# Performance work log

Measured on AMD Instinct MI355X. Metric: run time of the kernel, lower is better.

## Reference

```python
import jax, jax.numpy as jnp
import numpy as np

H = W = 28
NUM_COUNTS = 10  # iteration counts 0..9, one per logit of determine_n


def conv2d(x, w, b=None, pad=2):
    # x: [B,C,H,W], w: [O,I,5,5]
    y = jax.lax.conv_general_dilated(
        x, w, window_strides=(1, 1), padding=[(pad, pad), (pad, pad)],
        dimension_numbers=("NCHW", "OIHW", "NCHW"))
    if b is not None:
        y = y + b[None, :, None, None]
    return y


def maxpool3(x):
    # kernel 3, stride 3, valid: 28 -> 9
    return jax.lax.reduce_window(
        x, -jnp.inf, jax.lax.max,
        window_dimensions=(1, 1, 3, 3), window_strides=(1, 1, 3, 3),
        padding="VALID")


def setup_inputs() -> dict:
    key = jax.random.key(0)
    ks = jax.random.split(key, 8)
    B = 4096
    s = 0.1
    return {
        "x": jax.random.normal(ks[0], (B, H * W), dtype=jnp.float32),
        "w1": jax.random.normal(ks[1], (8, 1, 5, 5), dtype=jnp.float32) * s,
        "b1": jax.random.normal(ks[2], (8,), dtype=jnp.float32) * s,
        "w2": jax.random.normal(ks[3], (16, 8, 5, 5), dtype=jnp.float32) * s,
        "b2": jax.random.normal(ks[4], (16,), dtype=jnp.float32) * s,
        "fcw": jax.random.normal(ks[5], (10, 16 * 9 * 9), dtype=jnp.float32) * s,
        "fcb": jax.random.normal(ks[6], (10,), dtype=jnp.float32) * s,
        "iterw": jax.random.normal(ks[7], (1, 1, 5, 5), dtype=jnp.float32) * s,
    }


def reference(x, w1, b1, w2, b2, fcw, fcb, iterw):
    B = x.shape[0]
    xi = x.reshape(B, 1, H, W)
    # determine_n: CNN router producing 10 logits over iteration counts
    h = jax.nn.relu(conv2d(xi, w1, b1))
    h = jax.nn.relu(conv2d(h, w2, b2))
    h = maxpool3(h).reshape(B, -1)                      # [B, 1296]
    logits = h @ fcw.T + fcb                            # [B, 10]
    probs = jax.nn.softmax(logits, axis=-1)             # [B, 10]
    # smooth TmIter: expected value over f^n(base), n = 0..9
    def step(y, _):
        return conv2d(y, iterw, None), y
    _, ys = jax.lax.scan(step, xi, None, length=NUM_COUNTS)  # [10,B,1,28,28]
    out = jnp.einsum("bn,nbchw->bchw", probs, ys)
    return out.reshape(B, H, W)
```

## Files before the change

kernel.cpp:

```cpp
#include <hip/hip_runtime.h>
#include <hip/hip_bf16.h>
#include <math.h>
#include <float.h>

typedef __fp16 f16x8  __attribute__((ext_vector_type(8)));
typedef float  f32x16 __attribute__((ext_vector_type(16)));
typedef float  f32x4  __attribute__((ext_vector_type(4)));
typedef float  f32x2  __attribute__((ext_vector_type(2)));

#define DY_TAB 0xA524A509A502A540ULL
#define DX_TAB 0x446A444A44924924ULL

__global__ __launch_bounds__(256, 4) void k1_router(
    const float* __restrict__ xg,
    const float* __restrict__ w1g,
    const float* __restrict__ b1g,
    const float* __restrict__ w2g,
    const float* __restrict__ b2g,
    const float* __restrict__ fcwg,
    const float* __restrict__ fcbg,
    float* __restrict__ wsp)
{
    __shared__ __align__(16) char lds[28528];
    float*  spad   = (float*)(lds + 0);
    __fp16* sh1T   = (__fp16*)(lds + 4608);
    __fp16* sw2t   = (__fp16*)(lds + 21968);
    float*  pooled = (float*)(lds + 21968);
    float*  swred  = (float*)(lds + 28368);

    const int tid  = threadIdx.x;
    const int b    = blockIdx.x;
    const int lane = tid & 63;
    const int wid  = tid >> 6;

    const int ct = wid * 49 + lane;
    const int yy = ct / 7, q = ct - yy * 7;

    f32x4 z4 = {0.f, 0.f, 0.f, 0.f};
    for (int i = tid; i < 92; i += 256) {
        int row, cu;
        if (i < 36) { int r = i / 9; cu = i - 9 * r; row = r < 2 ? r : 28 + r; }
        else        { int j = i - 36; row = 2 + (j >> 1); cu = (j & 1) << 3; }
        ((f32x4*)spad)[row * 9 + cu] = z4;
    }
    for (int i = tid; i < 189; i += 256) {
        int row, col;
        if (i < 105) { int r = i / 35; row = (r == 2) ? 30 : r; col = i - 35 * r; }
        else         { int j = i - 105; row = 2 + j / 3; int cm = j - 3 * (j / 3);
                       col = (cm == 2) ? 30 : cm; }
        ((f32x4*)sh1T)[row * 35 + col] = z4;
    }
    for (int i = tid; i < 400; i += 256) {
        const int tap = i >> 4, ch = i & 15;
        f16x8 v;
        #pragma unroll
        for (int j = 0; j < 8; ++j) v[j] = (__fp16)w2g[ch * 200 + j * 25 + tap];
        *((f16x8*)(sw2t + i * 8)) = v;
    }
    if (lane < 49) {
        f32x4 v = *((const f32x4*)(xg + (size_t)b * 784 + yy * 28 + q * 4));
        *((f32x4*)(spad + (yy + 2) * 36 + q * 4 + 4)) = v;
    }
    __syncthreads();

    if (lane < 49) {
        float o[8][4];
        #pragma unroll
        for (int c = 0; c < 8; ++c) {
            const float bv = b1g[c];
            #pragma unroll
            for (int px = 0; px < 4; ++px) o[c][px] = bv;
        }
        #pragma unroll
        for (int r = 0; r < 5; ++r) {
            const float* rowp = spad + (yy + r) * 36 + q * 4;
            f32x4 a0 = ((const f32x4*)rowp)[0];
            f32x4 a1 = ((const f32x4*)rowp)[1];
            f32x4 a2 = ((const f32x4*)rowp)[2];
            float u[12] = {a0[0],a0[1],a0[2],a0[3], a1[0],a1[1],a1[2],a1[3],
                           a2[0],a2[1],a2[2],a2[3]};
            #pragma unroll
            for (int c = 0; c < 8; ++c)
                #pragma unroll
                for (int kx = 0; kx < 5; ++kx) {
                    const float w = w1g[c * 25 + r * 5 + kx];
                    #pragma unroll
                    for (int px = 0; px < 4; ++px)
                        o[c][px] = fmaf(u[2 + px + kx], w, o[c][px]);
                }
        }
        #pragma unroll
        for (int px = 0; px < 4; ++px) {
            f16x8 hv;
            #pragma unroll
            for (int c = 0; c < 8; ++c) hv[c] = (__fp16)fmaxf(o[c][px], 0.f);
            *((f16x8*)(sh1T + ((yy + 2) * 35 + (q * 4 + px + 2)) * 8)) = hv;
        }
    }
    const int lr = lane & 31;
    const int g2 = lane >> 5;
    int band = (lr * 57) >> 9; band = band > 2 ? 2 : band;
    const int dy = (int)((DY_TAB >> (2 * lr)) & 3ull);
    const int dx = (int)((DX_TAB >> (2 * lr)) & 3ull);
    const float biasv = (lr < 16) ? b2g[lr] : 0.f;

    f16x8 bfrag[13];
    int   toffB[13];
    #pragma unroll
    for (int s = 0; s < 13; ++s) {
        const int tap = 2 * s + g2;
        const int tapc = tap > 24 ? 24 : tap;
        f16x8 v = *((const f16x8*)(sw2t + (tapc * 16 + (lr & 15)) * 8));
        if (tap > 24 || lr >= 16) {
            #pragma unroll
            for (int j = 0; j < 8; ++j) v[j] = (__fp16)0.f;
        }
        bfrag[s] = v;
        const int ky = (tapc * 13) >> 6;
        const int kx = tapc - 5 * ky;
        toffB[s] = (ky * 35 + kx) * 16;
    }
    __syncthreads();

    for (int tile = wid; tile < 27; tile += 4) {
        const int cell = tile * 3 + band;
        const int cy = (cell * 57) >> 9, cx = cell - 9 * cy;
        const int R0 = 3 * cy + dy, C0 = 3 * cx + dx;
        const char* abase = (const char*)sh1T + (R0 * 35 + C0) * 16;
        f32x16 acc;
        #pragma unroll
        for (int r = 0; r < 16; ++r) acc[r] = biasv;
        #pragma unroll
        for (int s = 0; s < 13; ++s) {
            f16x8 af = *((const f16x8*)(abase + toffB[s]));
            acc = __builtin_amdgcn_mfma_f32_32x32x16_f16(af, bfrag[s], acc, 0, 0, 0);
        }
        float mA, mB, mC;
        if (g2 == 0) {
            mA = fmaxf(fmaxf(fmaxf(acc[0],acc[1]),fmaxf(acc[2],acc[3])), acc[4]);
            mB = fmaxf(fmaxf(fmaxf(acc[5],acc[6]),acc[7]), fmaxf(acc[8],acc[9]));
            mC = fmaxf(fmaxf(fmaxf(acc[10],acc[11]),acc[12]), fmaxf(acc[13],acc[14]));
        } else {
            mA = fmaxf(fmaxf(acc[0],acc[1]),fmaxf(acc[2],acc[3]));
            mB = fmaxf(fmaxf(acc[4],acc[5]),fmaxf(acc[6],acc[7]));
            mC = fmaxf(fmaxf(acc[8],acc[9]),fmaxf(acc[10],acc[11]));
        }
        mA = fmaxf(mA, 0.f); mB = fmaxf(mB, 0.f); mC = fmaxf(mC, 0.f);
        mA = fmaxf(mA, __shfl_xor(mA, 32, 64));
        mB = fmaxf(mB, __shfl_xor(mB, 32, 64));
        mC = fmaxf(mC, __shfl_xor(mC, 32, 64));
        if (g2 == 0 && lr < 16) {
            pooled[lr * 81 + tile * 3 + 0] = mA;
            pooled[lr * 81 + tile * 3 + 1] = mB;
            pooled[lr * 81 + tile * 3 + 2] = mC;
        }
    }
    __syncthreads();

    {
        float part[10];
        #pragma unroll
        for (int j = 0; j < 10; ++j) part[j] = 0.f;
        const int i4e = wid * 81 + 81;
        for (int i4 = wid * 81 + lane; i4 < i4e; i4 += 64) {
            const f32x4 pv = ((const f32x4*)pooled)[i4];
            #pragma unroll
            for (int j = 0; j < 10; ++j) {
                const f32x4 fw = *((const f32x4*)(fcwg + j * 1296 + i4 * 4));
                part[j] = fmaf(pv[0], fw[0], part[j]);
                part[j] = fmaf(pv[1], fw[1], part[j]);
                part[j] = fmaf(pv[2], fw[2], part[j]);
                part[j] = fmaf(pv[3], fw[3], part[j]);
            }
        }
        #pragma unroll
        for (int j = 0; j < 10; ++j) {
            float v = part[j];
            #pragma unroll
            for (int off = 32; off > 0; off >>= 1) v += __shfl_down(v, off, 64);
            if (lane == 0) swred[wid * 10 + j] = v;
        }
    }
    __syncthreads();

    if (tid == 0) {
        float lg[10]; float mx = -FLT_MAX;
        #pragma unroll
        for (int j = 0; j < 10; ++j) {
            lg[j] = swred[j] + swred[10 + j] + swred[20 + j] + swred[30 + j] + fcbg[j];
            mx = fmaxf(mx, lg[j]);
        }
        float sum = 0.f; float e[10];
        #pragma unroll
        for (int j = 0; j < 10; ++j) { e[j] = expf(lg[j] - mx); sum += e[j]; }
        const float inv = 1.f / sum;
        #pragma unroll
        for (int j = 0; j < 10; ++j) wsp[(size_t)b * 16 + j] = e[j] * inv;
    }
}

typedef __fp16 f16x2  __attribute__((ext_vector_type(2)));
typedef unsigned int u32x2 __attribute__((ext_vector_type(2)));

__device__ inline f16x2 as_h2(unsigned u) { union { unsigned x; f16x2 h; } c; c.x = u; return c.h; }
__device__ inline unsigned pack2(float lo, float hi) {
    union { f16x2 h; unsigned x; } c; c.h[0] = (__fp16)lo; c.h[1] = (__fp16)hi; return c.x;
}
__device__ inline float dot2f(unsigned a, unsigned b, float acc) {
#if __has_builtin(__builtin_amdgcn_fdot2)
    return __builtin_amdgcn_fdot2(as_h2(a), as_h2(b), acc, false);
#else
    f16x2 ah = as_h2(a), bh = as_h2(b);
    return fmaf((float)ah[1], (float)bh[1], fmaf((float)ah[0], (float)bh[0], acc));
#endif
}
#define ALIGN16(hi, lo) __builtin_amdgcn_alignbit((hi), (lo), 16)

__global__ __launch_bounds__(64, 4) void k2_scan(
    const float* __restrict__ xg,
    const float* __restrict__ iwg,
    const float* __restrict__ wsp,
    float* __restrict__ outg)
{
    __shared__ __align__(16) char arena[5120];
    char* bufA = arena;
    char* bufB = arena + 2560;

    const int tid = threadIdx.x;
    const int b   = blockIdx.x;

    f32x4 z4 = {0.f, 0.f, 0.f, 0.f};
    for (int i = tid; i < 320; i += 64) ((f32x4*)arena)[i] = z4;
    __syncthreads();

    for (int i = tid; i < 196; i += 64) {
        const int yy = i / 7, q = i - yy * 7;
        f32x4 v = *((const f32x4*)(xg + (size_t)b * 784 + yy * 28 + q * 4));
        unsigned* dst = (unsigned*)(bufA + (yy + 2) * 80 + q * 8 + 4);
        dst[0] = pack2(v[0], v[1]); dst[1] = pack2(v[2], v[3]);
    }
    __syncthreads();

    unsigned wp[5][3];
    #pragma unroll
    for (int r = 0; r < 5; ++r) {
        wp[r][0] = pack2(iwg[r * 5 + 0], iwg[r * 5 + 1]);
        wp[r][1] = pack2(iwg[r * 5 + 2], iwg[r * 5 + 3]);
        wp[r][2] = pack2(iwg[r * 5 + 4], 0.f);
    }

    const int rq = tid / 7, qq = tid - rq * 7;
    const float p0 = wsp[(size_t)b * 16];
    float accv[16];
    #pragma unroll
    for (int i = 0; i < 16; ++i) accv[i] = 0.f;

    const char* cur = bufA;
    char* nxt = bufB;
    #pragma unroll 1
    for (int n = 1; n <= 9; ++n) {
        const float pn = wsp[(size_t)b * 16 + n];
        if (tid < 49) {
            float v[4][4];
            #pragma unroll
            for (int rr = 0; rr < 4; ++rr)
                #pragma unroll
                for (int px = 0; px < 4; ++px) v[rr][px] = 0.f;
            #pragma unroll
            for (int r = 0; r < 8; ++r) {
                const char* rowb = cur + (4 * rq + r) * 80 + qq * 8;
                u32x2 A = *((const u32x2*)rowb);
                u32x2 B = *((const u32x2*)(rowb + 8));
                unsigned C0 = *((const unsigned*)(rowb + 16));
                unsigned P[8] = { A.x, ALIGN16(A.y, A.x), A.y, ALIGN16(B.x, A.y),
                                  B.x, ALIGN16(B.y, B.x), B.y, ALIGN16(C0,  B.y) };
                if (n == 1 && r >= 2 && r <= 5) {
                    f16x2 t1 = as_h2(A.y), t2 = as_h2(B.x);
                    accv[(r - 2) * 4 + 0] = p0 * (float)t1[0];
                    accv[(r - 2) * 4 + 1] = p0 * (float)t1[1];
                    accv[(r - 2) * 4 + 2] = p0 * (float)t2[0];
                    accv[(r - 2) * 4 + 3] = p0 * (float)t2[1];
                }
                #pragma unroll
                for (int rr = 0; rr < 4; ++rr) {
                    if (rr <= r && r <= rr + 4) {
                        const int ky = r - rr;
                        #pragma unroll
                        for (int px = 0; px < 4; ++px) {
                            float t = v[rr][px];
                            t = dot2f(P[px],     wp[ky][0], t);
                            t = dot2f(P[px + 2], wp[ky][1], t);
                            t = dot2f(P[px + 4], wp[ky][2], t);
                            v[rr][px] = t;
                        }
                    }
                }
            }
            if (n < 9) {
                #pragma unroll
                for (int rr = 0; rr < 4; ++rr) {
                    unsigned* dst = (unsigned*)(nxt + (4 * rq + rr + 2) * 80 + qq * 8 + 4);
                    dst[0] = pack2(v[rr][0], v[rr][1]);
                    dst[1] = pack2(v[rr][2], v[rr][3]);
                }
            }
            #pragma unroll
            for (int rr = 0; rr < 4; ++rr)
                #pragma unroll
                for (int px = 0; px < 4; ++px)
                    accv[rr * 4 + px] = fmaf(pn, v[rr][px], accv[rr * 4 + px]);
        }
        if (n < 9) __syncthreads();
        const char* t = cur; cur = nxt; nxt = (char*)t;
    }

    if (tid < 49) {
        #pragma unroll
        for (int rr = 0; rr < 4; ++rr) {
            f32x4 o = {accv[rr*4], accv[rr*4+1], accv[rr*4+2], accv[rr*4+3]};
            *((f32x4*)(outg + (size_t)b * 784 + (4 * rq + rr) * 28 + qq * 4)) = o;
        }
    }
}

extern "C" void kernel_launch(void* const* d_in, const int* in_sizes, int n_in,
                              void* d_out, int out_size, void* d_ws, size_t ws_size,
                              hipStream_t stream) {
    const float* x   = (const float*)d_in[0];
    const float* w1  = (const float*)d_in[1];
    const float* b1  = (const float*)d_in[2];
    const float* w2  = (const float*)d_in[3];
    const float* b2  = (const float*)d_in[4];
    const float* fcw = (const float*)d_in[5];
    const float* fcb = (const float*)d_in[6];
    const float* iw  = (const float*)d_in[7];
    float* out = (float*)d_out;
    float* wsp = (float*)d_ws;
    const int B = in_sizes[0] / 784;
    k1_router<<<B, 256, 0, stream>>>(x, w1, b1, w2, b2, fcw, fcb, wsp);
    k2_scan<<<B, 64, 0, stream>>>(x, iw, wsp, out);
}
```

Before: 113.8 us.

## Fuse router and iterative-conv scan into a single kernel

Merges the CNN router kernel and the 10-step iterated-convolution kernel into one 256-thread kernel per sample. The softmax probabilities now stay in shared memory instead of going through a global workspace, and the scan's input image is packed from the router's already-staged LDS copy rather than reloaded from global memory. This removes one kernel launch and the global round-trip. In exchange, the scan phase runs inside a 256-thread block where only the first wave does useful work, and each block holds the router's larger LDS footprint, which may lower occupancy during the scan.

```diff
diff --git a/kernel.cpp b/kernel.cpp
--- a/kernel.cpp
+++ b/kernel.cpp
@@ -4,202 +4,9 @@
 #include <float.h>
 
 typedef __fp16 f16x8  __attribute__((ext_vector_type(8)));
+typedef __fp16 f16x2  __attribute__((ext_vector_type(2)));
 typedef float  f32x16 __attribute__((ext_vector_type(16)));
 typedef float  f32x4  __attribute__((ext_vector_type(4)));
-typedef float  f32x2  __attribute__((ext_vector_type(2)));
-
-#define DY_TAB 0xA524A509A502A540ULL
-#define DX_TAB 0x446A444A44924924ULL
-
-__global__ __launch_bounds__(256, 4) void k1_router(
-    const float* __restrict__ xg,
-    const float* __restrict__ w1g,
-    const float* __restrict__ b1g,
-    const float* __restrict__ w2g,
-    const float* __restrict__ b2g,
-    const float* __restrict__ fcwg,
-    const float* __restrict__ fcbg,
-    float* __restrict__ wsp)
-{
-    __shared__ __align__(16) char lds[28528];
-    float*  spad   = (float*)(lds + 0);
-    __fp16* sh1T   = (__fp16*)(lds + 4608);
-    __fp16* sw2t   = (__fp16*)(lds + 21968);
-    float*  pooled = (float*)(lds + 21968);
-    float*  swred  = (float*)(lds + 28368);
-
-    const int tid  = threadIdx.x;
-    const int b    = blockIdx.x;
-    const int lane = tid & 63;
-    const int wid  = tid >> 6;
-
-    const int ct = wid * 49 + lane;
-    const int yy = ct / 7, q = ct - yy * 7;
-
-    f32x4 z4 = {0.f, 0.f, 0.f, 0.f};
-    for (int i = tid; i < 92; i += 256) {
-        int row, cu;
-        if (i < 36) { int r = i / 9; cu = i - 9 * r; row = r < 2 ? r : 28 + r; }
-        else        { int j = i - 36; row = 2 + (j >> 1); cu = (j & 1) << 3; }
-        ((f32x4*)spad)[row * 9 + cu] = z4;
-    }
-    for (int i = tid; i < 189; i += 256) {
-        int row, col;
-        if (i < 105) { int r = i / 35; row = (r == 2) ? 30 : r; col = i - 35 * r; }
-        else         { int j = i - 105; row = 2 + j / 3; int cm = j - 3 * (j / 3);
-                       col = (cm == 2) ? 30 : cm; }
-        ((f32x4*)sh1T)[row * 35 + col] = z4;
-    }
-    for (int i = tid; i < 400; i += 256) {
-        const int tap = i >> 4, ch = i & 15;
-        f16x8 v;
-        #pragma unroll
-        for (int j = 0; j < 8; ++j) v[j] = (__fp16)w2g[ch * 200 + j * 25 + tap];
-        *((f16x8*)(sw2t + i * 8)) = v;
-    }
-    if (lane < 49) {
-        f32x4 v = *((const f32x4*)(xg + (size_t)b * 784 + yy * 28 + q * 4));
-        *((f32x4*)(spad + (yy + 2) * 36 + q * 4 + 4)) = v;
-    }
-    __syncthreads();
-
-    if (lane < 49) {
-        float o[8][4];
-        #pragma unroll
-        for (int c = 0; c < 8; ++c) {
-            const float bv = b1g[c];
-            #pragma unroll
-            for (int px = 0; px < 4; ++px) o[c][px] = bv;
-        }
-        #pragma unroll
-        for (int r = 0; r < 5; ++r) {
-            const float* rowp = spad + (yy + r) * 36 + q * 4;
-            f32x4 a0 = ((const f32x4*)rowp)[0];
-            f32x4 a1 = ((const f32x4*)rowp)[1];
-            f32x4 a2 = ((const f32x4*)rowp)[2];
-            float u[12] = {a0[0],a0[1],a0[2],a0[3], a1[0],a1[1],a1[2],a1[3],
-                           a2[0],a2[1],a2[2],a2[3]};
-            #pragma unroll
-            for (int c = 0; c < 8; ++c)
-                #pragma unroll
-                for (int kx = 0; kx < 5; ++kx) {
-                    const float w = w1g[c * 25 + r * 5 + kx];
-                    #pragma unroll
-                    for (int px = 0; px < 4; ++px)
-                        o[c][px] = fmaf(u[2 + px + kx], w, o[c][px]);
-                }
-        }
-        #pragma unroll
-        for (int px = 0; px < 4; ++px) {
-            f16x8 hv;
-            #pragma unroll
-            for (int c = 0; c < 8; ++c) hv[c] = (__fp16)fmaxf(o[c][px], 0.f);
-            *((f16x8*)(sh1T + ((yy + 2) * 35 + (q * 4 + px + 2)) * 8)) = hv;
-        }
-    }
-    const int lr = lane & 31;
-    const int g2 = lane >> 5;
-    int band = (lr * 57) >> 9; band = band > 2 ? 2 : band;
-    const int dy = (int)((DY_TAB >> (2 * lr)) & 3ull);
-    const int dx = (int)((DX_TAB >> (2 * lr)) & 3ull);
-    const float biasv = (lr < 16) ? b2g[lr] : 0.f;
-
-    f16x8 bfrag[13];
-    int   toffB[13];
-    #pragma unroll
-    for (int s = 0; s < 13; ++s) {
-        const int tap = 2 * s + g2;
-        const int tapc = tap > 24 ? 24 : tap;
-        f16x8 v = *((const f16x8*)(sw2t + (tapc * 16 + (lr & 15)) * 8));
-        if (tap > 24 || lr >= 16) {
-            #pragma unroll
-            for (int j = 0; j < 8; ++j) v[j] = (__fp16)0.f;
-        }
-        bfrag[s] = v;
-        const int ky = (tapc * 13) >> 6;
-        const int kx = tapc - 5 * ky;
-        toffB[s] = (ky * 35 + kx) * 16;
-    }
-    __syncthreads();
-
-    for (int tile = wid; tile < 27; tile += 4) {
-        const int cell = tile * 3 + band;
-        const int cy = (cell * 57) >> 9, cx = cell - 9 * cy;
-        const int R0 = 3 * cy + dy, C0 = 3 * cx + dx;
-        const char* abase = (const char*)sh1T + (R0 * 35 + C0) * 16;
-        f32x16 acc;
-        #pragma unroll
-        for (int r = 0; r < 16; ++r) acc[r] = biasv;
-        #pragma unroll
-        for (int s = 0; s < 13; ++s) {
-            f16x8 af = *((const f16x8*)(abase + toffB[s]));
-            acc = __builtin_amdgcn_mfma_f32_32x32x16_f16(af, bfrag[s], acc, 0, 0, 0);
-        }
-        float mA, mB, mC;
-        if (g2 == 0) {
-            mA = fmaxf(fmaxf(fmaxf(acc[0],acc[1]),fmaxf(acc[2],acc[3])), acc[4]);
-            mB = fmaxf(fmaxf(fmaxf(acc[5],acc[6]),acc[7]), fmaxf(acc[8],acc[9]));
-            mC = fmaxf(fmaxf(fmaxf(acc[10],acc[11]),acc[12]), fmaxf(acc[13],acc[14]));
-        } else {
-            mA = fmaxf(fmaxf(acc[0],acc[1]),fmaxf(acc[2],acc[3]));
-            mB = fmaxf(fmaxf(acc[4],acc[5]),fmaxf(acc[6],acc[7]));
-            mC = fmaxf(fmaxf(acc[8],acc[9]),fmaxf(acc[10],acc[11]));
-        }
-        mA = fmaxf(mA, 0.f); mB = fmaxf(mB, 0.f); mC = fmaxf(mC, 0.f);
-        mA = fmaxf(mA, __shfl_xor(mA, 32, 64));
-        mB = fmaxf(mB, __shfl_xor(mB, 32, 64));
-        mC = fmaxf(mC, __shfl_xor(mC, 32, 64));
-        if (g2 == 0 && lr < 16) {
-            pooled[lr * 81 + tile * 3 + 0] = mA;
-            pooled[lr * 81 + tile * 3 + 1] = mB;
-            pooled[lr * 81 + tile * 3 + 2] = mC;
-        }
-    }
-    __syncthreads();
-
-    {
-        float part[10];
-        #pragma unroll
-        for (int j = 0; j < 10; ++j) part[j] = 0.f;
-        const int i4e = wid * 81 + 81;
-        for (int i4 = wid * 81 + lane; i4 < i4e; i4 += 64) {
-            const f32x4 pv = ((const f32x4*)pooled)[i4];
-            #pragma unroll
-            for (int j = 0; j < 10; ++j) {
-                const f32x4 fw = *((const f32x4*)(fcwg + j * 1296 + i4 * 4));
-                part[j] = fmaf(pv[0], fw[0], part[j]);
-                part[j] = fmaf(pv[1], fw[1], part[j]);
-                part[j] = fmaf(pv[2], fw[2], part[j]);
-                part[j] = fmaf(pv[3], fw[3], part[j]);
-            }
-        }
-        #pragma unroll
-        for (int j = 0; j < 10; ++j) {
-            float v = part[j];
-            #pragma unroll
-            for (int off = 32; off > 0; off >>= 1) v += __shfl_down(v, off, 64);
-            if (lane == 0) swred[wid * 10 + j] = v;
-        }
-    }
-    __syncthreads();
-
-    if (tid == 0) {
-        float lg[10]; float mx = -FLT_MAX;
-        #pragma unroll
-        for (int j = 0; j < 10; ++j) {
-            lg[j] = swred[j] + swred[10 + j] + swred[20 + j] + swred[30 + j] + fcbg[j];
-            mx = fmaxf(mx, lg[j]);
-        }
-        float sum = 0.f; float e[10];
-        #pragma unroll
-        for (int j = 0; j < 10; ++j) { e[j] = expf(lg[j] - mx); sum += e[j]; }
-        const float inv = 1.f / sum;
-        #pragma unroll
-        for (int j = 0; j < 10; ++j) wsp[(size_t)b * 16 + j] = e[j] * inv;
-    }
-}
-
-typedef __fp16 f16x2  __attribute__((ext_vector_type(2)));
 typedef unsigned int u32x2 __attribute__((ext_vector_type(2)));
 
 __device__ inline f16x2 as_h2(unsigned u) { union { unsigned x; f16x2 h; } c; c.x = u; return c.h; }
@@ -216,28 +23,206 @@
 }
 #define ALIGN16(hi, lo) __builtin_amdgcn_alignbit((hi), (lo), 16)
 
-__global__ __launch_bounds__(64, 4) void k2_scan(
+#define DY_TAB 0xA524A509A502A540ULL
+#define DX_TAB 0x446A444A44924924ULL
+
+__global__ __launch_bounds__(256, 4) void fused(
     const float* __restrict__ xg,
+    const float* __restrict__ w1g,
+    const float* __restrict__ b1g,
+    const float* __restrict__ w2g,
+    const float* __restrict__ b2g,
+    const float* __restrict__ fcwg,
+    const float* __restrict__ fcbg,
     const float* __restrict__ iwg,
-    const float* __restrict__ wsp,
     float* __restrict__ outg)
 {
-    __shared__ __align__(16) char arena[5120];
-    char* bufA = arena;
-    char* bufB = arena + 2560;
-
-    const int tid = threadIdx.x;
-    const int b   = blockIdx.x;
+    __shared__ __align__(16) char lds[28528];
+    float*  spad   = (float*)(lds + 0);
+    __fp16* sh1T   = (__fp16*)(lds + 4608);
+    char*   scanA  = lds + 4608;
+    char*   scanB  = lds + 7168;
+    __fp16* sw2t   = (__fp16*)(lds + 21968);
+    float*  pooled = (float*)(lds + 21968);
+    float*  swred  = (float*)(lds + 28368);
+
+    const int tid  = threadIdx.x;
+    const int b    = blockIdx.x;
+    const int lane = tid & 63;
+    const int wid  = tid >> 6;
+
+    const int ct = wid * 49 + lane;
+    const int yy = ct / 7, q = ct - yy * 7;
 
     f32x4 z4 = {0.f, 0.f, 0.f, 0.f};
-    for (int i = tid; i < 320; i += 64) ((f32x4*)arena)[i] = z4;
-    __syncthreads();
-
-    for (int i = tid; i < 196; i += 64) {
-        const int yy = i / 7, q = i - yy * 7;
+    for (int i = tid; i < 92; i += 256) {
+        int row, cu;
+        if (i < 36) { int r = i / 9; cu = i - 9 * r; row = r < 2 ? r : 28 + r; }
+        else        { int j = i - 36; row = 2 + (j >> 1); cu = (j & 1) << 3; }
+        ((f32x4*)spad)[row * 9 + cu] = z4;
+    }
+    for (int i = tid; i < 189; i += 256) {
+        int row, col;
+        if (i < 105) { int r = i / 35; row = (r == 2) ? 30 : r; col = i - 35 * r; }
+        else         { int j = i - 105; row = 2 + j / 3; int cm = j - 3 * (j / 3);
+                       col = (cm == 2) ? 30 : cm; }
+        ((f32x4*)sh1T)[row * 35 + col] = z4;
+    }
+    for (int i = tid; i < 400; i += 256) {
+        const int tap = i >> 4, ch = i & 15;
+        f16x8 v;
+        #pragma unroll
+        for (int j = 0; j < 8; ++j) v[j] = (__fp16)w2g[ch * 200 + j * 25 + tap];
+        *((f16x8*)(sw2t + i * 8)) = v;
+    }
+    if (lane < 49) {
         f32x4 v = *((const f32x4*)(xg + (size_t)b * 784 + yy * 28 + q * 4));
-        unsigned* dst = (unsigned*)(bufA + (yy + 2) * 80 + q * 8 + 4);
+        *((f32x4*)(spad + (yy + 2) * 36 + q * 4 + 4)) = v;
+    }
+    __syncthreads();
+
+    if (lane < 49) {
+        float o[8][4];
+        #pragma unroll
+        for (int c = 0; c < 8; ++c) {
+            const float bv = b1g[c];
+            #pragma unroll
+            for (int px = 0; px < 4; ++px) o[c][px] = bv;
+        }
+        #pragma unroll
+        for (int r = 0; r < 5; ++r) {
+            const float* rowp = spad + (yy + r) * 36 + q * 4;
+            f32x4 a0 = ((const f32x4*)rowp)[0];
+            f32x4 a1 = ((const f32x4*)rowp)[1];
+            f32x4 a2 = ((const f32x4*)rowp)[2];
+            float u[12] = {a0[0],a0[1],a0[2],a0[3], a1[0],a1[1],a1[2],a1[3],
+                           a2[0],a2[1],a2[2],a2[3]};
+            #pragma unroll
+            for (int c = 0; c < 8; ++c)
+                #pragma unroll
+                for (int kx = 0; kx < 5; ++kx) {
+                    const float w = w1g[c * 25 + r * 5 + kx];
+                    #pragma unroll
+                    for (int px = 0; px < 4; ++px)
+                        o[c][px] = fmaf(u[2 + px + kx], w, o[c][px]);
+                }
+        }
+        #pragma unroll
+        for (int px = 0; px < 4; ++px) {
+            f16x8 hv;
+            #pragma unroll
+            for (int c = 0; c < 8; ++c) hv[c] = (__fp16)fmaxf(o[c][px], 0.f);
+            *((f16x8*)(sh1T + ((yy + 2) * 35 + (q * 4 + px + 2)) * 8)) = hv;
+        }
+    }
+    const int lr = lane & 31;
+    const int g2 = lane >> 5;
+    int band = (lr * 57) >> 9; band = band > 2 ? 2 : band;
+    const int dy = (int)((DY_TAB >> (2 * lr)) & 3ull);
+    const int dx = (int)((DX_TAB >> (2 * lr)) & 3ull);
+    const float biasv = (lr < 16) ? b2g[lr] : 0.f;
+
+    f16x8 bfrag[13];
+    int   toffB[13];
+    #pragma unroll
+    for (int s = 0; s < 13; ++s) {
+        const int tap = 2 * s + g2;
+        const int tapc = tap > 24 ? 24 : tap;
+        f16x8 v = *((const f16x8*)(sw2t + (tapc * 16 + (lr & 15)) * 8));
+        if (tap > 24 || lr >= 16) {
+            #pragma unroll
+            for (int j = 0; j < 8; ++j) v[j] = (__fp16)0.f;
+        }
+        bfrag[s] = v;
+        const int ky = (tapc * 13) >> 6;
+        const int kx = tapc - 5 * ky;
+        toffB[s] = (ky * 35 + kx) * 16;
+    }
+    __syncthreads();
+
+    for (int tile = wid; tile < 27; tile += 4) {
+        const int cell = tile * 3 + band;
+        const int cy = (cell * 57) >> 9, cx = cell - 9 * cy;
+        const int R0 = 3 * cy + dy, C0 = 3 * cx + dx;
+        const char* abase = (const char*)sh1T + (R0 * 35 + C0) * 16;
+        f32x16 acc;
+        #pragma unroll
+        for (int r = 0; r < 16; ++r) acc[r] = biasv;
+        #pragma unroll
+        for (int s = 0; s < 13; ++s) {
+            f16x8 af = *((const f16x8*)(abase + toffB[s]));
+            acc = __builtin_amdgcn_mfma_f32_32x32x16_f16(af, bfrag[s], acc, 0, 0, 0);
+        }
+        float mA, mB, mC;
+        if (g2 == 0) {
+            mA = fmaxf(fmaxf(fmaxf(acc[0],acc[1]),fmaxf(acc[2],acc[3])), acc[4]);
+            mB = fmaxf(fmaxf(fmaxf(acc[5],acc[6]),acc[7]), fmaxf(acc[8],acc[9]));
+            mC = fmaxf(fmaxf(fmaxf(acc[10],acc[11]),acc[12]), fmaxf(acc[13],acc[14]));
+        } else {
+            mA = fmaxf(fmaxf(acc[0],acc[1]),fmaxf(acc[2],acc[3]));
+            mB = fmaxf(fmaxf(acc[4],acc[5]),fmaxf(acc[6],acc[7]));
+            mC = fmaxf(fmaxf(acc[8],acc[9]),fmaxf(acc[10],acc[11]));
+        }
+        mA = fmaxf(mA, 0.f); mB = fmaxf(mB, 0.f); mC = fmaxf(mC, 0.f);
+        mA = fmaxf(mA, __shfl_xor(mA, 32, 64));
+        mB = fmaxf(mB, __shfl_xor(mB, 32, 64));
+        mC = fmaxf(mC, __shfl_xor(mC, 32, 64));
+        if (g2 == 0 && lr < 16) {
+            pooled[lr * 81 + tile * 3 + 0] = mA;
+            pooled[lr * 81 + tile * 3 + 1] = mB;
+            pooled[lr * 81 + tile * 3 + 2] = mC;
+        }
+    }
+    __syncthreads();
+
+    for (int i = tid; i < 320; i += 256) {
+        ((f32x4*)scanA)[i] = z4;
+        if (i + 256 < 320 || tid < 64) {}
+    }
+    {
+        float part[10];
+        #pragma unroll
+        for (int j = 0; j < 10; ++j) part[j] = 0.f;
+        const int i4e = wid * 81 + 81;
+        for (int i4 = wid * 81 + lane; i4 < i4e; i4 += 64) {
+            const f32x4 pv = ((const f32x4*)pooled)[i4];
+            #pragma unroll
+            for (int j = 0; j < 10; ++j) {
+                const f32x4 fw = *((const f32x4*)(fcwg + j * 1296 + i4 * 4));
+                part[j] = fmaf(pv[0], fw[0], part[j]);
+                part[j] = fmaf(pv[1], fw[1], part[j]);
+                part[j] = fmaf(pv[2], fw[2], part[j]);
+                part[j] = fmaf(pv[3], fw[3], part[j]);
+            }
+        }
+        #pragma unroll
+        for (int j = 0; j < 10; ++j) {
+            float v = part[j];
+            #pragma unroll
+            for (int off = 32; off > 0; off >>= 1) v += __shfl_down(v, off, 64);
+            if (lane == 0) swred[wid * 10 + j] = v;
+        }
+    }
+    __syncthreads();
+
+    if (lane < 49) {
+        f32x4 v = *((const f32x4*)(spad + (yy + 2) * 36 + q * 4 + 4));
+        unsigned* dst = (unsigned*)(scanA + (yy + 2) * 80 + q * 8 + 4);
         dst[0] = pack2(v[0], v[1]); dst[1] = pack2(v[2], v[3]);
+    }
+    if (tid == 0) {
+        float lg[10]; float mx = -FLT_MAX;
+        #pragma unroll
+        for (int j = 0; j < 10; ++j) {
+            lg[j] = swred[j] + swred[10 + j] + swred[20 + j] + swred[30 + j] + fcbg[j];
+            mx = fmaxf(mx, lg[j]);
+        }
+        float sum = 0.f; float e[10];
+        #pragma unroll
+        for (int j = 0; j < 10; ++j) { e[j] = expf(lg[j] - mx); sum += e[j]; }
+        const float inv = 1.f / sum;
+        #pragma unroll
+        for (int j = 0; j < 10; ++j) swred[j] = e[j] * inv;
     }
     __syncthreads();
 
@@ -248,18 +233,17 @@
         wp[r][1] = pack2(iwg[r * 5 + 2], iwg[r * 5 + 3]);
         wp[r][2] = pack2(iwg[r * 5 + 4], 0.f);
     }
-
     const int rq = tid / 7, qq = tid - rq * 7;
-    const float p0 = wsp[(size_t)b * 16];
+    const float p0 = swred[0];
     float accv[16];
     #pragma unroll
     for (int i = 0; i < 16; ++i) accv[i] = 0.f;
 
-    const char* cur = bufA;
-    char* nxt = bufB;
+    const char* cur = scanA;
+    char* nxt = scanB;
     #pragma unroll 1
     for (int n = 1; n <= 9; ++n) {
-        const float pn = wsp[(size_t)b * 16 + n];
+        const float pn = swred[n];
         if (tid < 49) {
             float v[4][4];
             #pragma unroll
@@ -335,8 +319,6 @@
     const float* fcb = (const float*)d_in[6];
     const float* iw  = (const float*)d_in[7];
     float* out = (float*)d_out;
-    float* wsp = (float*)d_ws;
     const int B = in_sizes[0] / 784;
-    k1_router<<<B, 256, 0, stream>>>(x, w1, b1, w2, b2, fcw, fcb, wsp);
-    k2_scan<<<B, 64, 0, stream>>>(x, iw, wsp, out);
+    fused<<<B, 256, 0, stream>>>(x, w1, b1, w2, b2, fcw, fcb, iw, out);
 }
```

Measured after the change: 141.6 us. 24.4% more time.
